# Kernel optimization log

Hardware: AMD Instinct MI355X
Metric: run time of the kernel (lower is better)

## Reference

```python
import jax, jax.numpy as jnp
import numpy as np

# Norse LIFRefracParameters defaults
DT = 0.001
TAU_SYN_INV = 200.0
TAU_MEM_INV = 100.0
V_LEAK = 0.0
V_TH = 1.0
V_RESET = 0.0
ALPHA = 100.0          # super-spike surrogate slope
RHO_RESET = 5.0        # refractory steps after a spike
TAU_FILTER_INV = 223.1435511314

T, B, F, H, O = 1000, 64, 128, 512, 32


def heaviside(x):
    return (x > 0).astype(x.dtype)


def setup_inputs() -> dict:
    key = jax.random.key(0)
    k1, k2, k3, k4, k5 = jax.random.split(key, 5)
    x = jax.random.normal(k1, (T, B, F), dtype=jnp.float32)
    # torch Linear-style uniform(-1/sqrt(fan_in), 1/sqrt(fan_in)) init
    w_in = jax.random.uniform(k2, (H, F), jnp.float32, -1.0 / np.sqrt(F), 1.0 / np.sqrt(F))
    w_rec = jax.random.uniform(k3, (H, H), jnp.float32, -1.0 / np.sqrt(H), 1.0 / np.sqrt(H))
    w_out = jax.random.uniform(k4, (O, H), jnp.float32, -1.0 / np.sqrt(H), 1.0 / np.sqrt(H))
    b_out = jax.random.uniform(k5, (O,), jnp.float32, -1.0 / np.sqrt(H), 1.0 / np.sqrt(H))
    return {"x": x, "w_in": w_in, "w_rec": w_rec, "w_out": w_out, "b_out": b_out}


def reference(x, w_in, w_rec, w_out, b_out):
    Bd, Hd = x.shape[1], w_in.shape[0]

    def step(carry, x_t):
        z, v, i, rho, o = carry
        # LIF membrane/synapse Euler update (norse lif_step)
        v_dec = v + DT * TAU_MEM_INV * ((V_LEAK - v) + i)
        i_dec = i * (1.0 - DT * TAU_SYN_INV)
        z_new = heaviside(v_dec - V_TH)
        v_new = (1.0 - z_new) * v_dec + z_new * V_RESET
        i_new = i_dec + x_t @ w_in.T + z @ w_rec.T
        # refractory update (norse compute_refractory_update)
        refrac_mask = heaviside(rho)
        v_new = (1.0 - refrac_mask) * v_new + refrac_mask * v
        z_new = (1.0 - refrac_mask) * z_new
        rho_new = (1.0 - z_new) * jnp.maximum(rho - refrac_mask, 0.0) + z_new * RHO_RESET
        # ExpFilter: linear readout + exponential low-pass
        lin = z_new @ w_out.T + b_out
        o_new = o + DT * TAU_FILTER_INV * (lin - o)
        return (z_new, v_new, i_new, rho_new, o_new), o_new

    zeros_h = jnp.zeros((Bd, Hd), x.dtype)
    o0 = jnp.zeros((Bd, w_out.shape[0]), x.dtype)
    carry0 = (zeros_h, zeros_h, zeros_h, zeros_h, o0)
    _, outputs = jax.lax.scan(step, carry0, x)
    return outputs  # [T, B, O]
```

## Files before the change

### kernel.cpp

```cpp
#include <hip/hip_runtime.h>

#define T_STEPS 1000
#define BATCH   64
#define FIN     128
#define HID     512
#define NOUT    32
#define ALPHA_F 0.2231435511314f

__global__ void prep_transpose(const float* __restrict__ w_rec,
                               const float* __restrict__ w_out,
                               float* __restrict__ wrecT,
                               float* __restrict__ woutT) {
    int idx = blockIdx.x * blockDim.x + threadIdx.x;
    if (idx < HID * HID) {
        int j = idx / HID, h = idx % HID;
        wrecT[h * HID + j] = w_rec[idx];
    }
    if (idx < NOUT * HID) {
        int o = idx / HID, h = idx % HID;
        woutT[h * NOUT + o] = w_out[idx];
    }
}

#define GTM 128
#define GTN 128
#define GKC 32

__global__ __launch_bounds__(256)
void xwin_gemm(const float* __restrict__ x, const float* __restrict__ w_in,
               float* __restrict__ xwin) {
    __shared__ float xs[GKC][GTM + 4];
    __shared__ float ws[GKC][GTN + 4];
    const int tid = threadIdx.x;
    const int tb_base = blockIdx.x * GTM;
    const int h_base  = blockIdx.y * GTN;
    const int tx = tid & 15, ty = tid >> 4;

    float acc[8][8];
#pragma unroll
    for (int i = 0; i < 8; ++i)
#pragma unroll
        for (int j = 0; j < 8; ++j) acc[i][j] = 0.f;

    for (int kc = 0; kc < FIN; kc += GKC) {
#pragma unroll
        for (int q = 0; q < 4; ++q) {
            int li  = tid * 4 + q;
            int row = li >> 3, c4 = li & 7;
            float4 v = *(const float4*)&x[(size_t)(tb_base + row) * FIN + kc + c4 * 4];
            xs[c4*4+0][row] = v.x; xs[c4*4+1][row] = v.y;
            xs[c4*4+2][row] = v.z; xs[c4*4+3][row] = v.w;
            float4 w = *(const float4*)&w_in[(size_t)(h_base + row) * FIN + kc + c4 * 4];
            ws[c4*4+0][row] = w.x; ws[c4*4+1][row] = w.y;
            ws[c4*4+2][row] = w.z; ws[c4*4+3][row] = w.w;
        }
        __syncthreads();
#pragma unroll
        for (int k = 0; k < GKC; ++k) {
            float4 a0 = *(const float4*)&xs[k][tx * 8];
            float4 a1 = *(const float4*)&xs[k][tx * 8 + 4];
            float4 b0 = *(const float4*)&ws[k][ty * 8];
            float4 b1 = *(const float4*)&ws[k][ty * 8 + 4];
            float av[8] = {a0.x, a0.y, a0.z, a0.w, a1.x, a1.y, a1.z, a1.w};
            float bv[8] = {b0.x, b0.y, b0.z, b0.w, b1.x, b1.y, b1.z, b1.w};
#pragma unroll
            for (int i = 0; i < 8; ++i)
#pragma unroll
                for (int j = 0; j < 8; ++j)
                    acc[i][j] = fmaf(av[i], bv[j], acc[i][j]);
        }
        __syncthreads();
    }
#pragma unroll
    for (int i = 0; i < 8; ++i) {
        size_t tb = (size_t)tb_base + tx * 8 + i;
        float4 o0 = make_float4(acc[i][0], acc[i][1], acc[i][2], acc[i][3]);
        float4 o1 = make_float4(acc[i][4], acc[i][5], acc[i][6], acc[i][7]);
        *(float4*)&xwin[tb * HID + h_base + ty * 8]     = o0;
        *(float4*)&xwin[tb * HID + h_base + ty * 8 + 4] = o1;
    }
}

__global__ __launch_bounds__(64)
void snn_scan1w(const float* __restrict__ xwin,
                const float* __restrict__ wrT,
                unsigned long long* __restrict__ masks) {
    const int b    = blockIdx.x;
    const int lane = threadIdx.x;
    const size_t hoff = (size_t)lane * 8;

    float v[8], ic[8], rho[8];
    unsigned long long m[8];
#pragma unroll
    for (int j = 0; j < 8; ++j) { v[j] = 0.f; ic[j] = 0.f; rho[j] = 0.f; m[j] = 0ull; }

    const float* xrow0 = &xwin[(size_t)b * HID + hoff];
    float4 xa = *(const float4*)xrow0;
    float4 xb = *(const float4*)(xrow0 + 4);

    for (int t = 0; t < T_STEPS; ++t) {
        const int tn = (t + 1 < T_STEPS) ? t + 1 : t;
        const float* xnext = &xwin[((size_t)tn * BATCH + b) * HID + hoff];
        float4 xna = *(const float4*)xnext;
        float4 xnb = *(const float4*)(xnext + 4);

        float r[8];
#pragma unroll
        for (int j = 0; j < 8; ++j) r[j] = 0.f;
#pragma unroll
        for (int j = 0; j < 8; ++j) {
            unsigned long long mm = m[j];
            while (mm) {
                int l = (int)__builtin_ctzll(mm);
                mm &= mm - 1;
                const float* wp = &wrT[(size_t)(l * 8 + j) * HID + hoff];
                float4 wa = *(const float4*)wp;
                float4 wb = *(const float4*)(wp + 4);
                r[0] += wa.x; r[1] += wa.y; r[2] += wa.z; r[3] += wa.w;
                r[4] += wb.x; r[5] += wb.y; r[6] += wb.z; r[7] += wb.w;
            }
        }

        const float xi[8] = {xa.x, xa.y, xa.z, xa.w, xb.x, xb.y, xb.z, xb.w};
        float z[8];
#pragma unroll
        for (int j = 0; j < 8; ++j) {
            const float v_dec = v[j] + 0.1f * ((0.0f - v[j]) + ic[j]);
            const float i_dec = ic[j] * 0.8f;
            float zz     = (v_dec - 1.0f) > 0.0f ? 1.0f : 0.0f;
            float v_tmp  = (zz != 0.0f) ? 0.0f : v_dec;
            const float refr = (rho[j] > 0.0f) ? 1.0f : 0.0f;
            v[j]   = (refr != 0.0f) ? v[j] : v_tmp;
            zz     = (refr != 0.0f) ? 0.0f : zz;
            rho[j] = (zz != 0.0f) ? 5.0f : fmaxf(rho[j] - refr, 0.0f);
            ic[j]  = (i_dec + xi[j]) + r[j];
            z[j]   = zz;
        }
#pragma unroll
        for (int j = 0; j < 8; ++j) m[j] = __ballot(z[j] != 0.0f);

        if (lane == 0) {
            unsigned long long* mg = &masks[((size_t)t * BATCH + b) * 8];
#pragma unroll
            for (int j = 0; j < 8; ++j) mg[j] = m[j];
        }
        xa = xna; xb = xnb;
    }
}

__global__ __launch_bounds__(256)
void readout_lin(const unsigned long long* __restrict__ masks,
                 const float* __restrict__ woutT,
                 float* __restrict__ lin) {
    __shared__ float s_w[HID * NOUT];
    const int tid = threadIdx.x;
#pragma unroll
    for (int q = 0; q < 16; ++q) {
        int fi = (q * 256 + tid) * 4;
        int h = fi >> 5, o = fi & 31;
        float4 w = *(const float4*)&woutT[fi];
        int xs = (h & 7) << 2;
        *(float4*)&s_w[(h << 5) + (o ^ xs)] = w;
    }
    __syncthreads();

    const int b  = blockIdx.y;
    const int t  = blockIdx.x * 64 + (tid & 63);
    const int o0 = (tid >> 6) * 8;
    if (t >= T_STEPS) return;

    const unsigned long long* mp = &masks[((size_t)t * BATCH + b) * 8];
    float a0 = 0.f, a1 = 0.f, a2 = 0.f, a3 = 0.f, a4 = 0.f, a5 = 0.f, a6 = 0.f, a7 = 0.f;
#pragma unroll
    for (int j = 0; j < 8; ++j) {
        unsigned long long mm = mp[j];
        while (mm) {
            int l = (int)__builtin_ctzll(mm);
            mm &= mm - 1;
            int h  = l * 8 + j;
            int xs = (h & 7) << 2;
            const float4 w0 = *(const float4*)&s_w[(h << 5) + (o0 ^ xs)];
            const float4 w1 = *(const float4*)&s_w[(h << 5) + ((o0 + 4) ^ xs)];
            a0 += w0.x; a1 += w0.y; a2 += w0.z; a3 += w0.w;
            a4 += w1.x; a5 += w1.y; a6 += w1.z; a7 += w1.w;
        }
    }
    float* op = &lin[((size_t)t * BATCH + b) * NOUT + o0];
    *(float4*)op       = make_float4(a0, a1, a2, a3);
    *(float4*)(op + 4) = make_float4(a4, a5, a6, a7);
}

__global__ __launch_bounds__(256)
void readout_filter(const float* __restrict__ lin,
                    const float* __restrict__ b_out,
                    float* __restrict__ out) {
    const int bo = blockIdx.x * 256 + threadIdx.x;
    const int c  = blockIdx.y;
    const float bb = b_out[bo & 31];
    const int t0 = c * 125;
    int ts = t0 - 128; if (ts < 0) ts = 0;
    const int te = t0 + 125;
    float o = 0.f;
    for (int t = ts; t < te; ++t) {
        float l = lin[(size_t)t * (BATCH * NOUT) + bo] + bb;
        o = o + ALPHA_F * (l - o);
        if (t >= t0) out[(size_t)t * (BATCH * NOUT) + bo] = o;
    }
}

template<int PRECOMP>
__global__ __launch_bounds__(512)
void snn_main(const float* __restrict__ xsrc,
              const float* __restrict__ w_in,
              const float* __restrict__ wr, int wrA, int wrB,
              const float* __restrict__ wo, int woA, int woB,
              const float* __restrict__ b_out,
              float* __restrict__ out) {
    const int b    = blockIdx.x;
    const int tid  = threadIdx.x;
    const int lane = tid & 63;

    __shared__ int   s_list[2][HID];
    __shared__ int   s_cnt[2];
    __shared__ float s_xrow[2][FIN];

    if (tid < 2) s_cnt[tid] = 0;
    if (!PRECOMP && tid < FIN)
        s_xrow[0][tid] = xsrc[(size_t)b * FIN + tid];
    float iin_reg = 0.f;
    if (PRECOMP) iin_reg = xsrc[(size_t)b * HID + tid];
    __syncthreads();

    float v = 0.f, ic = 0.f, rho = 0.f, o_state = 0.f;
    const float bout_v = (tid < NOUT) ? b_out[tid] : 0.f;

    for (int t = 0; t < T_STEPS; ++t) {
        const int cur = t & 1, nxt = cur ^ 1;
        float iin_next = 0.f;
        if (PRECOMP) {
            int tn = (t + 1 < T_STEPS) ? (t + 1) : t;
            iin_next = xsrc[((size_t)tn * BATCH + b) * HID + tid];
        }
        float iin;
        if (PRECOMP) {
            iin = iin_reg;
        } else {
            float s0 = 0.f, s1 = 0.f, s2 = 0.f, s3 = 0.f;
#pragma unroll
            for (int kq = 0; kq < FIN / 4; ++kq) {
                float4 xv = *(const float4*)&s_xrow[cur][kq * 4];
                float4 wv = *(const float4*)&w_in[(size_t)tid * FIN + kq * 4];
                s0 = fmaf(xv.x, wv.x, s0); s1 = fmaf(xv.y, wv.y, s1);
                s2 = fmaf(xv.z, wv.z, s2); s3 = fmaf(xv.w, wv.w, s3);
            }
            iin = (s0 + s1) + (s2 + s3);
        }
        const int cn = s_cnt[cur];
        float r0 = 0.f, r1 = 0.f, r2 = 0.f, r3 = 0.f;
        int k = 0;
        for (; k + 4 <= cn; k += 4) {
            int i0 = s_list[cur][k],     i1 = s_list[cur][k + 1];
            int i2 = s_list[cur][k + 2], i3 = s_list[cur][k + 3];
            r0 += wr[(size_t)i0 * wrA + (size_t)tid * wrB];
            r1 += wr[(size_t)i1 * wrA + (size_t)tid * wrB];
            r2 += wr[(size_t)i2 * wrA + (size_t)tid * wrB];
            r3 += wr[(size_t)i3 * wrA + (size_t)tid * wrB];
        }
        for (; k < cn; ++k)
            r0 += wr[(size_t)s_list[cur][k] * wrA + (size_t)tid * wrB];
        const float rec = (r0 + r1) + (r2 + r3);

        const float v_dec = v + 0.1f * ((0.0f - v) + ic);
        const float i_dec = ic * 0.8f;
        float z      = (v_dec - 1.0f) > 0.0f ? 1.0f : 0.0f;
        float v_tmp  = (z != 0.0f) ? 0.0f : v_dec;
        const float refr = (rho > 0.0f) ? 1.0f : 0.0f;
        v   = (refr != 0.0f) ? v : v_tmp;
        z   = (refr != 0.0f) ? 0.0f : z;
        rho = (z != 0.0f) ? 5.0f : fmaxf(rho - refr, 0.0f);
        ic  = (i_dec + iin) + rec;

        unsigned long long mbal = __ballot(z != 0.0f);
        int nsp = __popcll(mbal);
        int base = 0;
        if (lane == 0 && nsp) base = atomicAdd(&s_cnt[nxt], nsp);
        base = __shfl(base, 0);
        if (z != 0.0f) {
            int pos = base + __popcll(mbal & ((1ull << lane) - 1ull));
            s_list[nxt][pos] = tid;
        }
        __syncthreads();

        if (tid < NOUT) {
            const int c2 = s_cnt[nxt];
            float lin = 0.f;
            for (int kk = 0; kk < c2; ++kk)
                lin += wo[(size_t)s_list[nxt][kk] * woA + (size_t)tid * woB];
            lin += bout_v;
            o_state = o_state + ALPHA_F * (lin - o_state);
            out[((size_t)t * BATCH + b) * NOUT + tid] = o_state;
        }
        if (tid == 0) s_cnt[cur] = 0;
        if (PRECOMP) iin_reg = iin_next;
        if (!PRECOMP && tid >= 128 && tid < 128 + FIN) {
            int tn = (t + 1 < T_STEPS) ? (t + 1) : t;
            s_xrow[nxt][tid - 128] = xsrc[((size_t)tn * BATCH + b) * FIN + (tid - 128)];
        }
        __syncthreads();
    }
}

extern "C" void kernel_launch(void* const* d_in, const int* in_sizes, int n_in,
                              void* d_out, int out_size, void* d_ws, size_t ws_size,
                              hipStream_t stream) {
    const float* x     = (const float*)d_in[0];
    const float* w_in  = (const float*)d_in[1];
    const float* w_rec = (const float*)d_in[2];
    const float* w_out = (const float*)d_in[3];
    const float* b_out = (const float*)d_in[4];
    float* out = (float*)d_out;

    const size_t xwin_b  = (size_t)T_STEPS * BATCH * HID * sizeof(float);
    const size_t masks_b = (size_t)T_STEPS * BATCH * 8 * sizeof(unsigned long long);
    const size_t wrect_b = (size_t)HID * HID * sizeof(float);
    const size_t woutt_b = (size_t)HID * NOUT * sizeof(float);

    char* ws = (char*)d_ws;

    if (ws_size >= xwin_b + masks_b + wrect_b + woutt_b) {
        float* xwin  = (float*)ws;
        float* lin   = (float*)ws;
        unsigned long long* masks = (unsigned long long*)(ws + xwin_b);
        float* wrecT = (float*)(ws + xwin_b + masks_b);
        float* woutT = (float*)(ws + xwin_b + masks_b + wrect_b);

        prep_transpose<<<(HID * HID + 255) / 256, 256, 0, stream>>>(w_rec, w_out, wrecT, woutT);
        dim3 g(T_STEPS * BATCH / GTM, HID / GTN);
        xwin_gemm<<<g, 256, 0, stream>>>(x, w_in, xwin);
        snn_scan1w<<<BATCH, 64, 0, stream>>>(xwin, wrecT, masks);
        readout_lin<<<dim3((T_STEPS + 63) / 64, BATCH), 256, 0, stream>>>(masks, woutT, lin);
        readout_filter<<<dim3(BATCH * NOUT / 256, 8), 256, 0, stream>>>(lin, b_out, out);
    } else if (ws_size >= xwin_b + wrect_b + woutt_b) {
        float* xwin  = (float*)ws;
        float* wrecT = (float*)(ws + xwin_b);
        float* woutT = (float*)(ws + xwin_b + wrect_b);
        prep_transpose<<<(HID * HID + 255) / 256, 256, 0, stream>>>(w_rec, w_out, wrecT, woutT);
        dim3 g(T_STEPS * BATCH / GTM, HID / GTN);
        xwin_gemm<<<g, 256, 0, stream>>>(x, w_in, xwin);
        snn_main<1><<<BATCH, HID, 0, stream>>>(xwin, nullptr, wrecT, HID, 1,
                                               woutT, NOUT, 1, b_out, out);
    } else if (ws_size >= wrect_b + woutt_b) {
        float* wrecT = (float*)ws;
        float* woutT = (float*)(ws + wrect_b);
        prep_transpose<<<(HID * HID + 255) / 256, 256, 0, stream>>>(w_rec, w_out, wrecT, woutT);
        snn_main<0><<<BATCH, HID, 0, stream>>>(x, w_in, wrecT, HID, 1,
                                               woutT, NOUT, 1, b_out, out);
    } else {
        snn_main<0><<<BATCH, HID, 0, stream>>>(x, w_in, w_rec, 1, HID,
                                               w_out, 1, HID, b_out, out);
    }
}
```

Baseline: 1.052 ms.

## Spread recurrent scan over four waves with shared-memory spike masks and batched gathers

Replaces the single-wave per-batch scan with a 256-thread block where each thread owns two hidden units and spike masks are exchanged through shared memory with a block barrier per step. The first two spikes per mask word are gathered unconditionally from a zero-padded extra row so loads can issue in parallel, and input projections are prefetched several steps ahead. The hidden-unit-to-mask-bit mapping changes to contiguous layout, so the readout indexing is updated to match. In exchange it adds a __syncthreads per timestep and up to 16 mostly-zero loads per step when spikes are sparse.

```diff
diff --git a/kernel.cpp b/kernel.cpp
--- a/kernel.cpp
+++ b/kernel.cpp
@@ -6,6 +6,8 @@
 #define HID     512
 #define NOUT    32
 #define ALPHA_F 0.2231435511314f
+#define PFD     4
+#define WREC_ROWS (HID + 8)
 
 __global__ void prep_transpose(const float* __restrict__ w_rec,
                                const float* __restrict__ w_out,
@@ -15,6 +17,8 @@
     if (idx < HID * HID) {
         int j = idx / HID, h = idx % HID;
         wrecT[h * HID + j] = w_rec[idx];
+    } else if (idx < HID * HID + 8 * HID) {
+        wrecT[idx] = 0.0f;
     }
     if (idx < NOUT * HID) {
         int o = idx / HID, h = idx % HID;
@@ -81,70 +85,129 @@
     }
 }
 
-__global__ __launch_bounds__(64)
-void snn_scan1w(const float* __restrict__ xwin,
+__global__ __launch_bounds__(256, 1)
+void snn_scan4w(const float* __restrict__ xwin,
                 const float* __restrict__ wrT,
                 unsigned long long* __restrict__ masks) {
     const int b    = blockIdx.x;
-    const int lane = threadIdx.x;
-    const size_t hoff = (size_t)lane * 8;
-
-    float v[8], ic[8], rho[8];
-    unsigned long long m[8];
-#pragma unroll
-    for (int j = 0; j < 8; ++j) { v[j] = 0.f; ic[j] = 0.f; rho[j] = 0.f; m[j] = 0ull; }
-
-    const float* xrow0 = &xwin[(size_t)b * HID + hoff];
-    float4 xa = *(const float4*)xrow0;
-    float4 xb = *(const float4*)(xrow0 + 4);
-
-    for (int t = 0; t < T_STEPS; ++t) {
-        const int tn = (t + 1 < T_STEPS) ? t + 1 : t;
-        const float* xnext = &xwin[((size_t)tn * BATCH + b) * HID + hoff];
-        float4 xna = *(const float4*)xnext;
-        float4 xnb = *(const float4*)(xnext + 4);
-
-        float r[8];
-#pragma unroll
-        for (int j = 0; j < 8; ++j) r[j] = 0.f;
-#pragma unroll
-        for (int j = 0; j < 8; ++j) {
-            unsigned long long mm = m[j];
-            while (mm) {
-                int l = (int)__builtin_ctzll(mm);
-                mm &= mm - 1;
-                const float* wp = &wrT[(size_t)(l * 8 + j) * HID + hoff];
-                float4 wa = *(const float4*)wp;
-                float4 wb = *(const float4*)(wp + 4);
-                r[0] += wa.x; r[1] += wa.y; r[2] += wa.z; r[3] += wa.w;
-                r[4] += wb.x; r[5] += wb.y; r[6] += wb.z; r[7] += wb.w;
-            }
-        }
-
-        const float xi[8] = {xa.x, xa.y, xa.z, xa.w, xb.x, xb.y, xb.z, xb.w};
-        float z[8];
-#pragma unroll
-        for (int j = 0; j < 8; ++j) {
-            const float v_dec = v[j] + 0.1f * ((0.0f - v[j]) + ic[j]);
-            const float i_dec = ic[j] * 0.8f;
-            float zz     = (v_dec - 1.0f) > 0.0f ? 1.0f : 0.0f;
-            float v_tmp  = (zz != 0.0f) ? 0.0f : v_dec;
-            const float refr = (rho[j] > 0.0f) ? 1.0f : 0.0f;
-            v[j]   = (refr != 0.0f) ? v[j] : v_tmp;
-            zz     = (refr != 0.0f) ? 0.0f : zz;
-            rho[j] = (zz != 0.0f) ? 5.0f : fmaxf(rho[j] - refr, 0.0f);
-            ic[j]  = (i_dec + xi[j]) + r[j];
-            z[j]   = zz;
-        }
-#pragma unroll
-        for (int j = 0; j < 8; ++j) m[j] = __ballot(z[j] != 0.0f);
-
-        if (lane == 0) {
-            unsigned long long* mg = &masks[((size_t)t * BATCH + b) * 8];
-#pragma unroll
-            for (int j = 0; j < 8; ++j) mg[j] = m[j];
-        }
-        xa = xna; xb = xnb;
+    const int tid  = threadIdx.x;
+    const int w    = tid >> 6;
+    const int lane = tid & 63;
+    const int h0 = tid, h1 = tid + 256;
+
+    __shared__ __align__(16) unsigned long long smasks[2][8];
+    if (tid < 16) ((unsigned long long*)smasks)[tid] = 0ull;
+    __syncthreads();
+
+    float v0 = 0.f, v1 = 0.f, c0 = 0.f, c1 = 0.f, q0 = 0.f, q1 = 0.f;
+
+    const float* wp0 = wrT + h0;
+    const float* wp1 = wrT + h1;
+
+    float xq0[PFD], xq1[PFD];
+#pragma unroll
+    for (int s = 0; s < PFD; ++s) {
+        xq0[s] = xwin[((size_t)s * BATCH + b) * HID + h0];
+        xq1[s] = xwin[((size_t)s * BATCH + b) * HID + h1];
+    }
+
+    for (int t0 = 0; t0 < T_STEPS; t0 += PFD) {
+        float pa0[PFD], pa1[PFD];
+#pragma unroll
+        for (int s = 0; s < PFD; ++s) {
+            int tn = t0 + PFD + s; if (tn >= T_STEPS) tn = T_STEPS - 1;
+            pa0[s] = xwin[((size_t)tn * BATCH + b) * HID + h0];
+            pa1[s] = xwin[((size_t)tn * BATCH + b) * HID + h1];
+        }
+
+#pragma unroll
+        for (int s = 0; s < PFD; ++s) {
+            const int t = t0 + s;
+            const int cur = t & 1, nxt = cur ^ 1;
+
+            const ulonglong2* sp = (const ulonglong2*)&smasks[cur][0];
+            ulonglong2 u0 = sp[0], u1 = sp[1], u2 = sp[2], u3 = sp[3];
+            unsigned long long wd[8] = {u0.x, u0.y, u1.x, u1.y,
+                                        u2.x, u2.y, u3.x, u3.y};
+
+            int rows[16];
+            unsigned long long rem[8];
+#pragma unroll
+            for (int j = 0; j < 8; ++j) {
+                unsigned long long u = wd[j];
+                int l0 = (u != 0ull) ? (int)__builtin_ctzll(u) : 64;
+                u &= u - 1;
+                int l1 = (u != 0ull) ? (int)__builtin_ctzll(u) : 64;
+                u &= u - 1;
+                rows[2 * j]     = (l0 < 64) ? (j * 64 + l0) : HID;
+                rows[2 * j + 1] = (l1 < 64) ? (j * 64 + l1) : HID;
+                rem[j] = u;
+            }
+
+            float g0[16], g1[16];
+#pragma unroll
+            for (int k = 0; k < 16; ++k) {
+                const size_t off = (size_t)rows[k] * HID;
+                g0[k] = wp0[off];
+                g1[k] = wp1[off];
+            }
+
+            float rec0 = (((g0[0]+g0[1])+(g0[2]+g0[3])) + ((g0[4]+g0[5])+(g0[6]+g0[7])))
+                       + (((g0[8]+g0[9])+(g0[10]+g0[11])) + ((g0[12]+g0[13])+(g0[14]+g0[15])));
+            float rec1 = (((g1[0]+g1[1])+(g1[2]+g1[3])) + ((g1[4]+g1[5])+(g1[6]+g1[7])))
+                       + (((g1[8]+g1[9])+(g1[10]+g1[11])) + ((g1[12]+g1[13])+(g1[14]+g1[15])));
+
+#pragma unroll
+            for (int j = 0; j < 8; ++j) {
+                while (rem[j]) {
+                    int l = (int)__builtin_ctzll(rem[j]);
+                    rem[j] &= rem[j] - 1;
+                    const size_t off = (size_t)(j * 64 + l) * HID;
+                    rec0 += wp0[off];
+                    rec1 += wp1[off];
+                }
+            }
+
+            float z0, z1;
+            {
+                const float v_dec = v0 + 0.1f * ((0.0f - v0) + c0);
+                const float i_dec = c0 * 0.8f;
+                float zz = (v_dec - 1.0f) > 0.0f ? 1.0f : 0.0f;
+                float v_tmp = (zz != 0.0f) ? 0.0f : v_dec;
+                const float refr = (q0 > 0.0f) ? 1.0f : 0.0f;
+                v0 = (refr != 0.0f) ? v0 : v_tmp;
+                zz = (refr != 0.0f) ? 0.0f : zz;
+                q0 = (zz != 0.0f) ? 5.0f : fmaxf(q0 - refr, 0.0f);
+                c0 = (i_dec + xq0[s]) + rec0;
+                z0 = zz;
+            }
+            {
+                const float v_dec = v1 + 0.1f * ((0.0f - v1) + c1);
+                const float i_dec = c1 * 0.8f;
+                float zz = (v_dec - 1.0f) > 0.0f ? 1.0f : 0.0f;
+                float v_tmp = (zz != 0.0f) ? 0.0f : v_dec;
+                const float refr = (q1 > 0.0f) ? 1.0f : 0.0f;
+                v1 = (refr != 0.0f) ? v1 : v_tmp;
+                zz = (refr != 0.0f) ? 0.0f : zz;
+                q1 = (zz != 0.0f) ? 5.0f : fmaxf(q1 - refr, 0.0f);
+                c1 = (i_dec + xq1[s]) + rec1;
+                z1 = zz;
+            }
+
+            const unsigned long long mA = __ballot(z0 != 0.0f);
+            const unsigned long long mB = __ballot(z1 != 0.0f);
+
+            if (lane == 0) {
+                smasks[nxt][w]     = mA;
+                smasks[nxt][4 + w] = mB;
+                unsigned long long* mg = &masks[((size_t)t * BATCH + b) * 8];
+                mg[w]     = mA;
+                mg[4 + w] = mB;
+            }
+            __syncthreads();
+        }
+#pragma unroll
+        for (int s = 0; s < PFD; ++s) { xq0[s] = pa0[s]; xq1[s] = pa1[s]; }
     }
 }
 
@@ -177,7 +240,7 @@
         while (mm) {
             int l = (int)__builtin_ctzll(mm);
             mm &= mm - 1;
-            int h  = l * 8 + j;
+            int h  = j * 64 + l;
             int xs = (h & 7) << 2;
             const float4 w0 = *(const float4*)&s_w[(h << 5) + (o0 ^ xs)];
             const float4 w1 = *(const float4*)&s_w[(h << 5) + ((o0 + 4) ^ xs)];
@@ -322,10 +385,11 @@
 
     const size_t xwin_b  = (size_t)T_STEPS * BATCH * HID * sizeof(float);
     const size_t masks_b = (size_t)T_STEPS * BATCH * 8 * sizeof(unsigned long long);
-    const size_t wrect_b = (size_t)HID * HID * sizeof(float);
+    const size_t wrect_b = (size_t)WREC_ROWS * HID * sizeof(float);
     const size_t woutt_b = (size_t)HID * NOUT * sizeof(float);
 
     char* ws = (char*)d_ws;
+    const int prep_n = HID * HID + 8 * HID;
 
     if (ws_size >= xwin_b + masks_b + wrect_b + woutt_b) {
         float* xwin  = (float*)ws;
@@ -334,17 +398,17 @@
         float* wrecT = (float*)(ws + xwin_b + masks_b);
         float* woutT = (float*)(ws + xwin_b + masks_b + wrect_b);
 
-        prep_transpose<<<(HID * HID + 255) / 256, 256, 0, stream>>>(w_rec, w_out, wrecT, woutT);
+        prep_transpose<<<(prep_n + 255) / 256, 256, 0, stream>>>(w_rec, w_out, wrecT, woutT);
         dim3 g(T_STEPS * BATCH / GTM, HID / GTN);
         xwin_gemm<<<g, 256, 0, stream>>>(x, w_in, xwin);
-        snn_scan1w<<<BATCH, 64, 0, stream>>>(xwin, wrecT, masks);
+        snn_scan4w<<<BATCH, 256, 0, stream>>>(xwin, wrecT, masks);
         readout_lin<<<dim3((T_STEPS + 63) / 64, BATCH), 256, 0, stream>>>(masks, woutT, lin);
         readout_filter<<<dim3(BATCH * NOUT / 256, 8), 256, 0, stream>>>(lin, b_out, out);
     } else if (ws_size >= xwin_b + wrect_b + woutt_b) {
         float* xwin  = (float*)ws;
         float* wrecT = (float*)(ws + xwin_b);
         float* woutT = (float*)(ws + xwin_b + wrect_b);
-        prep_transpose<<<(HID * HID + 255) / 256, 256, 0, stream>>>(w_rec, w_out, wrecT, woutT);
+        prep_transpose<<<(prep_n + 255) / 256, 256, 0, stream>>>(w_rec, w_out, wrecT, woutT);
         dim3 g(T_STEPS * BATCH / GTM, HID / GTN);
         xwin_gemm<<<g, 256, 0, stream>>>(x, w_in, xwin);
         snn_main<1><<<BATCH, HID, 0, stream>>>(xwin, nullptr, wrecT, HID, 1,
@@ -352,7 +416,7 @@
     } else if (ws_size >= wrect_b + woutt_b) {
         float* wrecT = (float*)ws;
         float* woutT = (float*)(ws + wrect_b);
-        prep_transpose<<<(HID * HID + 255) / 256, 256, 0, stream>>>(w_rec, w_out, wrecT, woutT);
+        prep_transpose<<<(prep_n + 255) / 256, 256, 0, stream>>>(w_rec, w_out, wrecT, woutT);
         snn_main<0><<<BATCH, HID, 0, stream>>>(x, w_in, wrecT, HID, 1,
                                                woutT, NOUT, 1, b_out, out);
     } else {
```

New measurement: 1.253 ms. 19.1% more time.
